# Performance work log

Hardware: AMD Instinct MI355X
Metric: run time of the kernel (lower is better)

The kernel has to match this reference:

```python
import jax, jax.numpy as jnp
import numpy as np

D_DIM = 128
K_DIM = 32


def setup_inputs() -> dict:
    key = jax.random.key(0)
    k1, k2, k3 = jax.random.split(key, 3)
    B, H, W = 8, 64, 64
    std1 = 1.0 / (K_DIM * D_DIM) ** 0.5
    std2 = 1.0 / K_DIM ** 0.5
    X = jax.random.normal(k1, (B, D_DIM, H, W), dtype=jnp.float32)
    codewords = jax.random.uniform(k2, (K_DIM, D_DIM), dtype=jnp.float32, minval=-std1, maxval=std1)
    scale = jax.random.uniform(k3, (K_DIM,), dtype=jnp.float32, minval=-std2, maxval=std2)
    return {"X": X, "codewords": codewords, "scale": scale}


def reference(X, codewords, scale):
    # X: [B, D, H, W] -> descriptors [B, N, D]
    B, D, H, W = X.shape
    Xf = X.reshape(B, D, H * W).transpose(0, 2, 1)  # [B, N, D]
    # Squared distance ||x - c||^2 expanded: avoids materializing [B,N,K,D]
    x_sq = jnp.sum(Xf * Xf, axis=-1, keepdims=True)          # [B, N, 1]
    c_sq = jnp.sum(codewords * codewords, axis=-1)           # [K]
    cross = jnp.einsum('bnd,kd->bnk', Xf, codewords)         # [B, N, K]
    dist2 = x_sq - 2.0 * cross + c_sq                        # [B, N, K]
    # NOTE: faithful to source -- softmax over scale * dist^2 (no negation)
    A = jax.nn.softmax(dist2 * scale, axis=-1)               # [B, N, K]
    # E[b,k,d] = sum_n A[b,n,k] * (x[b,n,d] - c[k,d])
    E = jnp.einsum('bnk,bnd->bkd', A, Xf) - jnp.sum(A, axis=1)[..., None] * codewords
    return E  # [B, K, D]
```

## Files before the change

kernel.cpp:

```cpp
#include <hip/hip_runtime.h>
#include <hip/hip_bf16.h>

#define D_DIM 128
#define K_DIM 32
#define NPIX  4096
#define TPB   128

typedef __bf16 bf16x8 __attribute__((ext_vector_type(8)));
typedef unsigned short u16x8 __attribute__((ext_vector_type(8)));
typedef float f32x4 __attribute__((ext_vector_type(4)));

__device__ __forceinline__ unsigned short f2bf(float f) {
    union { float f; unsigned u; } v; v.f = f;
    unsigned r = v.u + 0x7FFFu + ((v.u >> 16) & 1u);
    return (unsigned short)(r >> 16);
}
__device__ __forceinline__ unsigned pack2(float lo, float hi) {
    __hip_bfloat162 h = __float22bfloat162_rn(make_float2(lo, hi));
    union { __hip_bfloat162 b; unsigned u; } u; u.b = h;
    return u.u;
}
__device__ __forceinline__ float bf2f(unsigned short u) {
    union { unsigned u; float f; } v; v.u = ((unsigned)u) << 16;
    return v.f;
}
__device__ __forceinline__ bf16x8 ldfrag(const unsigned short* p) {
    union { u16x8 s; bf16x8 b; } u;
    u.s = *(const u16x8*)p;
    return u.b;
}
__device__ __forceinline__ bf16x8 pack8(float4 a, float4 b) {
    union { unsigned d[4]; bf16x8 v; } u;
    u.d[0] = pack2(a.x, a.y); u.d[1] = pack2(a.z, a.w);
    u.d[2] = pack2(b.x, b.y); u.d[3] = pack2(b.z, b.w);
    return u.v;
}

#define XND_LD 136
#define CW_LD  136
#define SA_LD  136

__global__ __launch_bounds__(512) void enc_kernel(
    const float* __restrict__ X,
    const float* __restrict__ cw,
    const float* __restrict__ scale,
    float* __restrict__ out)
{
    __shared__ __align__(16) unsigned short sXnd[TPB * XND_LD];
    __shared__ __align__(16) unsigned short sCW[K_DIM * CW_LD];
    __shared__ __align__(16) unsigned short sA[K_DIM * SA_LD];
    __shared__ float sXsqP[16 * 129];
    __shared__ float sXsq[TPB];
    __shared__ float sSum[K_DIM];
    __shared__ float sSc[K_DIM];
    __shared__ float sCS[K_DIM];

    const int ltid = threadIdx.x;
    const int b    = blockIdx.x >> 5;
    const int n0   = (blockIdx.x & 31) * TPB;
    const int lane = ltid & 63;
    const int w    = ltid >> 6;
    const int l15  = lane & 15;
    const int quad = lane >> 4;

    if (ltid < K_DIM) {
        const float4* cr = (const float4*)(cw + ltid * D_DIM);
        float cs = 0.f;
        #pragma unroll 8
        for (int q = 0; q < 32; ++q) {
            float4 c4 = cr[q];
            cs = fmaf(c4.x, c4.x, fmaf(c4.y, c4.y, fmaf(c4.z, c4.z, fmaf(c4.w, c4.w, cs))));
        }
        float s = scale[ltid];
        sSc[ltid] = s;
        sCS[ltid] = cs * s;
        sSum[ltid] = 0.f;
    }

    {
        const int r  = ltid >> 4;
        const int q8 = ltid & 15;
        float4 c0 = *(const float4*)(cw + r * D_DIM + 8 * q8);
        float4 c1 = *(const float4*)(cw + r * D_DIM + 8 * q8 + 4);
        uint4 pk;
        pk.x = pack2(c0.x, c0.y); pk.y = pack2(c0.z, c0.w);
        pk.z = pack2(c1.x, c1.y); pk.w = pack2(c1.z, c1.w);
        *(uint4*)&sCW[r * CW_LD + 8 * q8] = pk;
    }

    {
        const int c   = ltid & 15;
        const int rp  = (ltid >> 4) & 3;
        const int ph  = ltid >> 6;
        const int pxh = (ph & 1) * 64;
        const int dbl = (ph >> 1) * 16;
        float px[4] = {0.f, 0.f, 0.f, 0.f};
        const float* xb = X + (size_t)b * D_DIM * NPIX + n0 + pxh;
        #pragma unroll
        for (int p = 0; p < 4; ++p) {
            const int pair = rp + 4 * p + dbl;
            const int d0   = 2 * pair;
            float4 f0 = *(const float4*)(xb + (size_t)d0 * NPIX + 4 * c);
            float4 f1 = *(const float4*)(xb + (size_t)(d0 + 1) * NPIX + 4 * c);
            px[0] = fmaf(f0.x, f0.x, fmaf(f1.x, f1.x, px[0]));
            px[1] = fmaf(f0.y, f0.y, fmaf(f1.y, f1.y, px[1]));
            px[2] = fmaf(f0.z, f0.z, fmaf(f1.z, f1.z, px[2]));
            px[3] = fmaf(f0.w, f0.w, fmaf(f1.w, f1.w, px[3]));
            const int pix = pxh + 4 * c;
            *(unsigned*)&sXnd[(pix + 0) * XND_LD + d0] = pack2(f0.x, f1.x);
            *(unsigned*)&sXnd[(pix + 1) * XND_LD + d0] = pack2(f0.y, f1.y);
            *(unsigned*)&sXnd[(pix + 2) * XND_LD + d0] = pack2(f0.z, f1.z);
            *(unsigned*)&sXnd[(pix + 3) * XND_LD + d0] = pack2(f0.w, f1.w);
        }
        const int row = rp + 4 * (ph >> 1);
        #pragma unroll
        for (int j = 0; j < 4; ++j) sXsqP[row * 129 + pxh + 4 * c + j] = px[j];
    }

    float4 g[4][2];
    {
        const int d = 16 * w + l15;
        const float* xrow = X + ((size_t)b * D_DIM + d) * NPIX + n0;
        #pragma unroll
        for (int ks = 0; ks < 4; ++ks) {
            const float* p = xrow + 8 * quad + 32 * ks;
            g[ks][0] = *(const float4*)p;
            g[ks][1] = *(const float4*)(p + 4);
        }
    }
    __syncthreads();

    if (ltid < TPB) {
        float s = 0.f;
        #pragma unroll
        for (int r = 0; r < 16; ++r) s += sXsqP[r * 129 + ltid];
        sXsq[ltid] = s;
    }

    f32x4 accA[2] = {{0.f, 0.f, 0.f, 0.f}, {0.f, 0.f, 0.f, 0.f}};
    {
        const int prow = (16 * w + l15) * XND_LD;
        #pragma unroll
        for (int ks = 0; ks < 4; ++ks) {
            const int off = 8 * quad + 32 * ks;
            bf16x8 bfrag = ldfrag(&sXnd[prow + off]);
            bf16x8 a0 = ldfrag(&sCW[l15 * CW_LD + off]);
            bf16x8 a1 = ldfrag(&sCW[(l15 + 16) * CW_LD + off]);
            accA[0] = __builtin_amdgcn_mfma_f32_16x16x32_bf16(a0, bfrag, accA[0], 0, 0, 0);
            accA[1] = __builtin_amdgcn_mfma_f32_16x16x32_bf16(a1, bfrag, accA[1], 0, 0, 0);
        }
    }
    __syncthreads();

    {
        const float xsq = sXsq[16 * w + l15];
        float e8[8];
        float psum = 0.f;
        #pragma unroll
        for (int mt = 0; mt < 2; ++mt)
            #pragma unroll
            for (int reg = 0; reg < 4; ++reg) {
                const int k = 16 * mt + 4 * quad + reg;
                float l = fmaf(sSc[k], fmaf(-2.f, accA[mt][reg], xsq), sCS[k]);
                float e = __expf(l);
                e8[4 * mt + reg] = e;
                psum += e;
            }
        psum += __shfl_xor(psum, 16);
        psum += __shfl_xor(psum, 32);
        const float inv = 1.f / psum;
        float r8[8];
        #pragma unroll
        for (int i = 0; i < 8; ++i) {
            e8[i] *= inv;
            r8[i] = e8[i];
        }
        #pragma unroll
        for (int mt = 0; mt < 2; ++mt)
            #pragma unroll
            for (int reg = 0; reg < 4; ++reg) {
                const int k = 16 * mt + 4 * quad + reg;
                sA[k * SA_LD + 16 * w + l15] = f2bf(e8[4 * mt + reg]);
            }
        #pragma unroll
        for (int i = 0; i < 8; ++i) {
            r8[i] += __shfl_xor(r8[i], 1);
            r8[i] += __shfl_xor(r8[i], 2);
            r8[i] += __shfl_xor(r8[i], 4);
            r8[i] += __shfl_xor(r8[i], 8);
        }
        if (l15 == 0) {
            #pragma unroll
            for (int mt = 0; mt < 2; ++mt)
                #pragma unroll
                for (int reg = 0; reg < 4; ++reg)
                    atomicAdd(&sSum[16 * mt + 4 * quad + reg], r8[4 * mt + reg]);
        }
    }
    __syncthreads();

    f32x4 accE[2] = {{0.f, 0.f, 0.f, 0.f}, {0.f, 0.f, 0.f, 0.f}};
    {
        #pragma unroll
        for (int ks = 0; ks < 4; ++ks) {
            const int off = 8 * quad + 32 * ks;
            bf16x8 bfrag = pack8(g[ks][0], g[ks][1]);
            bf16x8 a0 = ldfrag(&sA[l15 * SA_LD + off]);
            bf16x8 a1 = ldfrag(&sA[(l15 + 16) * SA_LD + off]);
            accE[0] = __builtin_amdgcn_mfma_f32_16x16x32_bf16(a0, bfrag, accE[0], 0, 0, 0);
            accE[1] = __builtin_amdgcn_mfma_f32_16x16x32_bf16(a1, bfrag, accE[1], 0, 0, 0);
        }
    }

    {
        float* outb = out + (size_t)b * (K_DIM * D_DIM);
        const int d = 16 * w + l15;
        #pragma unroll
        for (int mt = 0; mt < 2; ++mt) {
            #pragma unroll
            for (int rr = 0; rr < 4; ++rr) {
                const int reg = (rr + blockIdx.x) & 3;
                const int k = 16 * mt + 4 * quad + reg;
                float sk  = sSum[k];
                float cwv = bf2f(sCW[k * CW_LD + d]);
                float v = fmaf(-sk, cwv, accE[mt][reg]);
                atomicAdd(outb + k * D_DIM + d, v);
            }
        }
    }
}

extern "C" void kernel_launch(void* const* d_in, const int* in_sizes, int n_in,
                              void* d_out, int out_size, void* d_ws, size_t ws_size,
                              hipStream_t stream) {
    const float* X  = (const float*)d_in[0];
    const float* cw = (const float*)d_in[1];
    const float* sc = (const float*)d_in[2];
    float* out = (float*)d_out;
    (void)in_sizes; (void)n_in; (void)d_ws; (void)ws_size; (void)out_size;

    hipLaunchKernelGGL(enc_kernel, dim3(256), dim3(512), 0, stream, X, cw, sc, out);
}
```

Measured before the change: 71.72 us.

## Halve block to 256 threads with two tiles per wave and deferred X reloads

Shrinks the workgroup from 512 to 256 threads, so each wave now handles two 16-pixel tiles in the distance MFMA and two 16-wide d tiles in the encoding MFMA. The staging loops are redistributed to match. The second-stage X loads are moved from before the first barrier to just before the E matmul, so they are no longer held in registers across the softmax. This aims to allow two blocks per CU, cut barrier cost, and reuse A and codeword fragments across more MFMAs. In exchange, per-thread work and register pressure rise, and the X reload latency is now exposed late in the kernel.

```diff
diff --git a/kernel.cpp b/kernel.cpp
--- a/kernel.cpp
+++ b/kernel.cpp
@@ -40,7 +40,7 @@
 #define CW_LD  136
 #define SA_LD  136
 
-__global__ __launch_bounds__(512) void enc_kernel(
+__global__ __launch_bounds__(256, 2) void enc_kernel(
     const float* __restrict__ X,
     const float* __restrict__ cw,
     const float* __restrict__ scale,
@@ -49,7 +49,7 @@
     __shared__ __align__(16) unsigned short sXnd[TPB * XND_LD];
     __shared__ __align__(16) unsigned short sCW[K_DIM * CW_LD];
     __shared__ __align__(16) unsigned short sA[K_DIM * SA_LD];
-    __shared__ float sXsqP[16 * 129];
+    __shared__ float sXsqP[8 * 129];
     __shared__ float sXsq[TPB];
     __shared__ float sSum[K_DIM];
     __shared__ float sSc[K_DIM];
@@ -78,110 +78,106 @@
     }
 
     {
-        const int r  = ltid >> 4;
-        const int q8 = ltid & 15;
-        float4 c0 = *(const float4*)(cw + r * D_DIM + 8 * q8);
-        float4 c1 = *(const float4*)(cw + r * D_DIM + 8 * q8 + 4);
-        uint4 pk;
-        pk.x = pack2(c0.x, c0.y); pk.y = pack2(c0.z, c0.w);
-        pk.z = pack2(c1.x, c1.y); pk.w = pack2(c1.z, c1.w);
-        *(uint4*)&sCW[r * CW_LD + 8 * q8] = pk;
-    }
-
-    {
-        const int c   = ltid & 15;
-        const int rp  = (ltid >> 4) & 3;
-        const int ph  = ltid >> 6;
-        const int pxh = (ph & 1) * 64;
-        const int dbl = (ph >> 1) * 16;
+        const int r  = ltid >> 3;
+        const int q8 = ltid & 7;
+        const float* cr = cw + r * D_DIM + 16 * q8;
+        float4 c0 = *(const float4*)(cr + 0);
+        float4 c1 = *(const float4*)(cr + 4);
+        float4 c2 = *(const float4*)(cr + 8);
+        float4 c3 = *(const float4*)(cr + 12);
+        uint4 p0, p1;
+        p0.x = pack2(c0.x, c0.y); p0.y = pack2(c0.z, c0.w);
+        p0.z = pack2(c1.x, c1.y); p0.w = pack2(c1.z, c1.w);
+        p1.x = pack2(c2.x, c2.y); p1.y = pack2(c2.z, c2.w);
+        p1.z = pack2(c3.x, c3.y); p1.w = pack2(c3.z, c3.w);
+        *(uint4*)&sCW[r * CW_LD + 16 * q8 + 0] = p0;
+        *(uint4*)&sCW[r * CW_LD + 16 * q8 + 8] = p1;
+    }
+
+    {
+        const int c = ltid & 31;
+        const int r = ltid >> 5;
         float px[4] = {0.f, 0.f, 0.f, 0.f};
-        const float* xb = X + (size_t)b * D_DIM * NPIX + n0 + pxh;
-        #pragma unroll
-        for (int p = 0; p < 4; ++p) {
-            const int pair = rp + 4 * p + dbl;
-            const int d0   = 2 * pair;
+        const float* xb = X + (size_t)b * D_DIM * NPIX + n0;
+        #pragma unroll
+        for (int p = 0; p < 8; ++p) {
+            const int d0 = 2 * (r + 8 * p);
             float4 f0 = *(const float4*)(xb + (size_t)d0 * NPIX + 4 * c);
             float4 f1 = *(const float4*)(xb + (size_t)(d0 + 1) * NPIX + 4 * c);
             px[0] = fmaf(f0.x, f0.x, fmaf(f1.x, f1.x, px[0]));
             px[1] = fmaf(f0.y, f0.y, fmaf(f1.y, f1.y, px[1]));
             px[2] = fmaf(f0.z, f0.z, fmaf(f1.z, f1.z, px[2]));
             px[3] = fmaf(f0.w, f0.w, fmaf(f1.w, f1.w, px[3]));
-            const int pix = pxh + 4 * c;
-            *(unsigned*)&sXnd[(pix + 0) * XND_LD + d0] = pack2(f0.x, f1.x);
-            *(unsigned*)&sXnd[(pix + 1) * XND_LD + d0] = pack2(f0.y, f1.y);
-            *(unsigned*)&sXnd[(pix + 2) * XND_LD + d0] = pack2(f0.z, f1.z);
-            *(unsigned*)&sXnd[(pix + 3) * XND_LD + d0] = pack2(f0.w, f1.w);
-        }
-        const int row = rp + 4 * (ph >> 1);
-        #pragma unroll
-        for (int j = 0; j < 4; ++j) sXsqP[row * 129 + pxh + 4 * c + j] = px[j];
-    }
-
-    float4 g[4][2];
-    {
-        const int d = 16 * w + l15;
-        const float* xrow = X + ((size_t)b * D_DIM + d) * NPIX + n0;
-        #pragma unroll
-        for (int ks = 0; ks < 4; ++ks) {
-            const float* p = xrow + 8 * quad + 32 * ks;
-            g[ks][0] = *(const float4*)p;
-            g[ks][1] = *(const float4*)(p + 4);
-        }
+            *(unsigned*)&sXnd[(4 * c + 0) * XND_LD + d0] = pack2(f0.x, f1.x);
+            *(unsigned*)&sXnd[(4 * c + 1) * XND_LD + d0] = pack2(f0.y, f1.y);
+            *(unsigned*)&sXnd[(4 * c + 2) * XND_LD + d0] = pack2(f0.z, f1.z);
+            *(unsigned*)&sXnd[(4 * c + 3) * XND_LD + d0] = pack2(f0.w, f1.w);
+        }
+        #pragma unroll
+        for (int j = 0; j < 4; ++j) sXsqP[r * 129 + 4 * c + j] = px[j];
     }
     __syncthreads();
 
     if (ltid < TPB) {
         float s = 0.f;
         #pragma unroll
-        for (int r = 0; r < 16; ++r) s += sXsqP[r * 129 + ltid];
+        for (int r = 0; r < 8; ++r) s += sXsqP[r * 129 + ltid];
         sXsq[ltid] = s;
     }
 
-    f32x4 accA[2] = {{0.f, 0.f, 0.f, 0.f}, {0.f, 0.f, 0.f, 0.f}};
-    {
-        const int prow = (16 * w + l15) * XND_LD;
+    f32x4 accA[2][2] = {{{0.f,0.f,0.f,0.f},{0.f,0.f,0.f,0.f}},
+                        {{0.f,0.f,0.f,0.f},{0.f,0.f,0.f,0.f}}};
+    {
+        const int prow0 = (32 * w + l15) * XND_LD;
+        const int prow1 = (32 * w + 16 + l15) * XND_LD;
         #pragma unroll
         for (int ks = 0; ks < 4; ++ks) {
             const int off = 8 * quad + 32 * ks;
-            bf16x8 bfrag = ldfrag(&sXnd[prow + off]);
             bf16x8 a0 = ldfrag(&sCW[l15 * CW_LD + off]);
             bf16x8 a1 = ldfrag(&sCW[(l15 + 16) * CW_LD + off]);
-            accA[0] = __builtin_amdgcn_mfma_f32_16x16x32_bf16(a0, bfrag, accA[0], 0, 0, 0);
-            accA[1] = __builtin_amdgcn_mfma_f32_16x16x32_bf16(a1, bfrag, accA[1], 0, 0, 0);
+            bf16x8 b0 = ldfrag(&sXnd[prow0 + off]);
+            bf16x8 b1 = ldfrag(&sXnd[prow1 + off]);
+            accA[0][0] = __builtin_amdgcn_mfma_f32_16x16x32_bf16(a0, b0, accA[0][0], 0, 0, 0);
+            accA[0][1] = __builtin_amdgcn_mfma_f32_16x16x32_bf16(a1, b0, accA[0][1], 0, 0, 0);
+            accA[1][0] = __builtin_amdgcn_mfma_f32_16x16x32_bf16(a0, b1, accA[1][0], 0, 0, 0);
+            accA[1][1] = __builtin_amdgcn_mfma_f32_16x16x32_bf16(a1, b1, accA[1][1], 0, 0, 0);
         }
     }
     __syncthreads();
 
     {
-        const float xsq = sXsq[16 * w + l15];
-        float e8[8];
-        float psum = 0.f;
-        #pragma unroll
-        for (int mt = 0; mt < 2; ++mt)
-            #pragma unroll
-            for (int reg = 0; reg < 4; ++reg) {
-                const int k = 16 * mt + 4 * quad + reg;
-                float l = fmaf(sSc[k], fmaf(-2.f, accA[mt][reg], xsq), sCS[k]);
-                float e = __expf(l);
-                e8[4 * mt + reg] = e;
-                psum += e;
+        float r8[8] = {0.f,0.f,0.f,0.f,0.f,0.f,0.f,0.f};
+        #pragma unroll
+        for (int pt = 0; pt < 2; ++pt) {
+            const float xsq = sXsq[32 * w + 16 * pt + l15];
+            float e8[8];
+            float psum = 0.f;
+            #pragma unroll
+            for (int mt = 0; mt < 2; ++mt)
+                #pragma unroll
+                for (int reg = 0; reg < 4; ++reg) {
+                    const int k = 16 * mt + 4 * quad + reg;
+                    float l = fmaf(sSc[k], fmaf(-2.f, accA[pt][mt][reg], xsq), sCS[k]);
+                    float e = __expf(l);
+                    e8[4 * mt + reg] = e;
+                    psum += e;
+                }
+            psum += __shfl_xor(psum, 16);
+            psum += __shfl_xor(psum, 32);
+            const float inv = 1.f / psum;
+            #pragma unroll
+            for (int i = 0; i < 8; ++i) {
+                e8[i] *= inv;
+                r8[i] += e8[i];
             }
-        psum += __shfl_xor(psum, 16);
-        psum += __shfl_xor(psum, 32);
-        const float inv = 1.f / psum;
-        float r8[8];
-        #pragma unroll
-        for (int i = 0; i < 8; ++i) {
-            e8[i] *= inv;
-            r8[i] = e8[i];
-        }
-        #pragma unroll
-        for (int mt = 0; mt < 2; ++mt)
-            #pragma unroll
-            for (int reg = 0; reg < 4; ++reg) {
-                const int k = 16 * mt + 4 * quad + reg;
-                sA[k * SA_LD + 16 * w + l15] = f2bf(e8[4 * mt + reg]);
-            }
+            #pragma unroll
+            for (int mt = 0; mt < 2; ++mt)
+                #pragma unroll
+                for (int reg = 0; reg < 4; ++reg) {
+                    const int k = 16 * mt + 4 * quad + reg;
+                    sA[k * SA_LD + 32 * w + 16 * pt + l15] = f2bf(e8[4 * mt + reg]);
+                }
+        }
         #pragma unroll
         for (int i = 0; i < 8; ++i) {
             r8[i] += __shfl_xor(r8[i], 1);
@@ -199,32 +195,46 @@
     }
     __syncthreads();
 
-    f32x4 accE[2] = {{0.f, 0.f, 0.f, 0.f}, {0.f, 0.f, 0.f, 0.f}};
-    {
+    f32x4 accE[2][2] = {{{0.f,0.f,0.f,0.f},{0.f,0.f,0.f,0.f}},
+                        {{0.f,0.f,0.f,0.f},{0.f,0.f,0.f,0.f}}};
+    #pragma unroll
+    for (int dt = 0; dt < 2; ++dt) {
+        const int d = 16 * (2 * w + dt) + l15;
+        const float* xrow = X + ((size_t)b * D_DIM + d) * NPIX + n0;
+        float4 g[4][2];
+        #pragma unroll
+        for (int ks = 0; ks < 4; ++ks) {
+            const float* p = xrow + 8 * quad + 32 * ks;
+            g[ks][0] = *(const float4*)p;
+            g[ks][1] = *(const float4*)(p + 4);
+        }
         #pragma unroll
         for (int ks = 0; ks < 4; ++ks) {
             const int off = 8 * quad + 32 * ks;
             bf16x8 bfrag = pack8(g[ks][0], g[ks][1]);
             bf16x8 a0 = ldfrag(&sA[l15 * SA_LD + off]);
             bf16x8 a1 = ldfrag(&sA[(l15 + 16) * SA_LD + off]);
-            accE[0] = __builtin_amdgcn_mfma_f32_16x16x32_bf16(a0, bfrag, accE[0], 0, 0, 0);
-            accE[1] = __builtin_amdgcn_mfma_f32_16x16x32_bf16(a1, bfrag, accE[1], 0, 0, 0);
+            accE[dt][0] = __builtin_amdgcn_mfma_f32_16x16x32_bf16(a0, bfrag, accE[dt][0], 0, 0, 0);
+            accE[dt][1] = __builtin_amdgcn_mfma_f32_16x16x32_bf16(a1, bfrag, accE[dt][1], 0, 0, 0);
         }
     }
 
     {
         float* outb = out + (size_t)b * (K_DIM * D_DIM);
-        const int d = 16 * w + l15;
-        #pragma unroll
-        for (int mt = 0; mt < 2; ++mt) {
-            #pragma unroll
-            for (int rr = 0; rr < 4; ++rr) {
-                const int reg = (rr + blockIdx.x) & 3;
-                const int k = 16 * mt + 4 * quad + reg;
-                float sk  = sSum[k];
-                float cwv = bf2f(sCW[k * CW_LD + d]);
-                float v = fmaf(-sk, cwv, accE[mt][reg]);
-                atomicAdd(outb + k * D_DIM + d, v);
+        #pragma unroll
+        for (int dt = 0; dt < 2; ++dt) {
+            const int d = 16 * (2 * w + dt) + l15;
+            #pragma unroll
+            for (int mt = 0; mt < 2; ++mt) {
+                #pragma unroll
+                for (int rr = 0; rr < 4; ++rr) {
+                    const int reg = (rr + blockIdx.x) & 3;
+                    const int k = 16 * mt + 4 * quad + reg;
+                    float sk  = sSum[k];
+                    float cwv = bf2f(sCW[k * CW_LD + d]);
+                    float v = fmaf(-sk, cwv, accE[dt][mt][reg]);
+                    atomicAdd(outb + k * D_DIM + d, v);
+                }
             }
         }
     }
@@ -239,5 +249,5 @@
     float* out = (float*)d_out;
     (void)in_sizes; (void)n_in; (void)d_ws; (void)ws_size; (void)out_size;
 
-    hipLaunchKernelGGL(enc_kernel, dim3(256), dim3(512), 0, stream, X, cw, sc, out);
-}
+    hipLaunchKernelGGL(enc_kernel, dim3(256), dim3(256), 0, stream, X, cw, sc, out);
+}
```

New measurement: 71.82 us. About the same (+0.1%).

## Transpose X into LDS with 16-byte swizzled stores and drop xsq barrier

Applied to the files above, without the earlier changes.

Each thread in the X staging phase now loads 8 consecutive channels for 4 pixels and writes packed 16-byte bf16 chunks into an XOR-swizzled LDS layout, replacing many 4-byte scattered stores. The MFMA B-fragment reads apply the matching swizzle. The separate pass that reduced the per-pixel squared norms into sXsq, and the barrier after it, are removed. Each lane now sums the 16 partials itself, trading redundant LDS reads for one fewer __syncthreads and fewer LDS store instructions with fewer bank conflicts.

```diff
diff --git a/kernel.cpp b/kernel.cpp
--- a/kernel.cpp
+++ b/kernel.cpp
@@ -50,7 +50,6 @@
     __shared__ __align__(16) unsigned short sCW[K_DIM * CW_LD];
     __shared__ __align__(16) unsigned short sA[K_DIM * SA_LD];
     __shared__ float sXsqP[16 * 129];
-    __shared__ float sXsq[TPB];
     __shared__ float sSum[K_DIM];
     __shared__ float sSc[K_DIM];
     __shared__ float sCS[K_DIM];
@@ -80,8 +79,9 @@
     {
         const int r  = ltid >> 4;
         const int q8 = ltid & 15;
-        float4 c0 = *(const float4*)(cw + r * D_DIM + 8 * q8);
-        float4 c1 = *(const float4*)(cw + r * D_DIM + 8 * q8 + 4);
+        const float* cr = cw + r * D_DIM + 8 * q8;
+        float4 c0 = *(const float4*)(cr + 0);
+        float4 c1 = *(const float4*)(cr + 4);
         uint4 pk;
         pk.x = pack2(c0.x, c0.y); pk.y = pack2(c0.z, c0.w);
         pk.z = pack2(c1.x, c1.y); pk.w = pack2(c1.z, c1.w);
@@ -89,32 +89,37 @@
     }
 
     {
-        const int c   = ltid & 15;
-        const int rp  = (ltid >> 4) & 3;
-        const int ph  = ltid >> 6;
-        const int pxh = (ph & 1) * 64;
-        const int dbl = (ph >> 1) * 16;
+        const int c = ltid & 31;
+        const int r = ltid >> 5;
         float px[4] = {0.f, 0.f, 0.f, 0.f};
-        const float* xb = X + (size_t)b * D_DIM * NPIX + n0 + pxh;
-        #pragma unroll
-        for (int p = 0; p < 4; ++p) {
-            const int pair = rp + 4 * p + dbl;
-            const int d0   = 2 * pair;
-            float4 f0 = *(const float4*)(xb + (size_t)d0 * NPIX + 4 * c);
-            float4 f1 = *(const float4*)(xb + (size_t)(d0 + 1) * NPIX + 4 * c);
-            px[0] = fmaf(f0.x, f0.x, fmaf(f1.x, f1.x, px[0]));
-            px[1] = fmaf(f0.y, f0.y, fmaf(f1.y, f1.y, px[1]));
-            px[2] = fmaf(f0.z, f0.z, fmaf(f1.z, f1.z, px[2]));
-            px[3] = fmaf(f0.w, f0.w, fmaf(f1.w, f1.w, px[3]));
-            const int pix = pxh + 4 * c;
-            *(unsigned*)&sXnd[(pix + 0) * XND_LD + d0] = pack2(f0.x, f1.x);
-            *(unsigned*)&sXnd[(pix + 1) * XND_LD + d0] = pack2(f0.y, f1.y);
-            *(unsigned*)&sXnd[(pix + 2) * XND_LD + d0] = pack2(f0.z, f1.z);
-            *(unsigned*)&sXnd[(pix + 3) * XND_LD + d0] = pack2(f0.w, f1.w);
-        }
-        const int row = rp + 4 * (ph >> 1);
-        #pragma unroll
-        for (int j = 0; j < 4; ++j) sXsqP[row * 129 + pxh + 4 * c + j] = px[j];
+        const float* xb = X + (size_t)b * D_DIM * NPIX + n0;
+        float fx[8], fy[8], fz[8], fw[8];
+        #pragma unroll
+        for (int dd = 0; dd < 8; ++dd) {
+            const int d = 8 * r + dd;
+            float4 f = *(const float4*)(xb + (size_t)d * NPIX + 4 * c);
+            fx[dd] = f.x; fy[dd] = f.y; fz[dd] = f.z; fw[dd] = f.w;
+            px[0] = fmaf(f.x, f.x, px[0]);
+            px[1] = fmaf(f.y, f.y, px[1]);
+            px[2] = fmaf(f.z, f.z, px[2]);
+            px[3] = fmaf(f.w, f.w, px[3]);
+        }
+        const int pchunk = ((r & 7) ^ (c & 7)) + (r & 8);
+        uint4 pk;
+        pk.x = pack2(fx[0], fx[1]); pk.y = pack2(fx[2], fx[3]);
+        pk.z = pack2(fx[4], fx[5]); pk.w = pack2(fx[6], fx[7]);
+        *(uint4*)&sXnd[(4 * c + 0) * XND_LD + 8 * pchunk] = pk;
+        pk.x = pack2(fy[0], fy[1]); pk.y = pack2(fy[2], fy[3]);
+        pk.z = pack2(fy[4], fy[5]); pk.w = pack2(fy[6], fy[7]);
+        *(uint4*)&sXnd[(4 * c + 1) * XND_LD + 8 * pchunk] = pk;
+        pk.x = pack2(fz[0], fz[1]); pk.y = pack2(fz[2], fz[3]);
+        pk.z = pack2(fz[4], fz[5]); pk.w = pack2(fz[6], fz[7]);
+        *(uint4*)&sXnd[(4 * c + 2) * XND_LD + 8 * pchunk] = pk;
+        pk.x = pack2(fw[0], fw[1]); pk.y = pack2(fw[2], fw[3]);
+        pk.z = pack2(fw[4], fw[5]); pk.w = pack2(fw[6], fw[7]);
+        *(uint4*)&sXnd[(4 * c + 3) * XND_LD + 8 * pchunk] = pk;
+        #pragma unroll
+        for (int j = 0; j < 4; ++j) sXsqP[r * 129 + 4 * c + j] = px[j];
     }
 
     float4 g[4][2];
@@ -130,30 +135,27 @@
     }
     __syncthreads();
 
-    if (ltid < TPB) {
-        float s = 0.f;
-        #pragma unroll
-        for (int r = 0; r < 16; ++r) s += sXsqP[r * 129 + ltid];
-        sXsq[ltid] = s;
-    }
-
     f32x4 accA[2] = {{0.f, 0.f, 0.f, 0.f}, {0.f, 0.f, 0.f, 0.f}};
     {
         const int prow = (16 * w + l15) * XND_LD;
+        const int xr   = (4 * w + (l15 >> 2)) & 7;
         #pragma unroll
         for (int ks = 0; ks < 4; ++ks) {
+            const int lg = quad + 4 * ks;
+            const int ph = ((lg & 7) ^ xr) + (lg & 8);
             const int off = 8 * quad + 32 * ks;
-            bf16x8 bfrag = ldfrag(&sXnd[prow + off]);
             bf16x8 a0 = ldfrag(&sCW[l15 * CW_LD + off]);
             bf16x8 a1 = ldfrag(&sCW[(l15 + 16) * CW_LD + off]);
-            accA[0] = __builtin_amdgcn_mfma_f32_16x16x32_bf16(a0, bfrag, accA[0], 0, 0, 0);
-            accA[1] = __builtin_amdgcn_mfma_f32_16x16x32_bf16(a1, bfrag, accA[1], 0, 0, 0);
-        }
-    }
-    __syncthreads();
-
-    {
-        const float xsq = sXsq[16 * w + l15];
+            bf16x8 bf = ldfrag(&sXnd[prow + 8 * ph]);
+            accA[0] = __builtin_amdgcn_mfma_f32_16x16x32_bf16(a0, bf, accA[0], 0, 0, 0);
+            accA[1] = __builtin_amdgcn_mfma_f32_16x16x32_bf16(a1, bf, accA[1], 0, 0, 0);
+        }
+    }
+
+    {
+        float xsq = 0.f;
+        #pragma unroll
+        for (int r = 0; r < 16; ++r) xsq += sXsqP[r * 129 + 16 * w + l15];
         float e8[8];
         float psum = 0.f;
         #pragma unroll
```

Result: no change. 72.31 us (+0.8%).
